# Kernel tuning notes

Hardware: AMD Instinct MI355X
Metric: run time of the kernel (lower is better)

The kernel has to match this reference:

```python
import jax, jax.numpy as jnp
import numpy as np

EPS = 1e-9
N_HEAD = 16


def clamp_c(c):
    return jnp.clip(c, 1e-4, 1.0)


def _heads(x, H):
    B, T, C = x.shape
    return x.reshape(B, T, H, C // H)


def mobius_add(x, y, c_clamped, H):
    # per-head Mobius addition; c_clamped: (H,)
    B, T, C = x.shape
    cr = c_clamped.reshape(1, 1, H, 1)
    xr, yr = _heads(x, H), _heads(y, H)
    xn = jnp.sum(xr * xr, axis=-1, keepdims=True)
    yn = jnp.sum(yr * yr, axis=-1, keepdims=True)
    ip = jnp.sum(xr * yr, axis=-1, keepdims=True)
    num = (1 + 2 * cr * ip + cr * yn) * xr + (1 - cr * xn) * yr
    den = 1 + 2 * cr * ip + cr ** 2 * xn * yn
    return (num / (den + EPS)).reshape(B, T, C)


def expmap(x, v, c, H):
    # exponential map of tangent vector v at point x (per-head curvature)
    B, T, C = x.shape
    cc = clamp_c(c)
    cr = cc.reshape(1, 1, H, 1)
    xr, vr = _heads(x, H), _heads(v, H)
    sf = 2.0 / (1 + cr * jnp.sum(xr * xr, axis=-1, keepdims=True) + EPS)  # scaling factor
    vns = jnp.sum(vr * vr, axis=-1, keepdims=True)
    vn = jnp.sqrt(vns + EPS)
    tanh_arg = jnp.abs(cr * sf * vns / 2)
    coeff = (1.0 / (jnp.sqrt(jnp.abs(cr) + EPS) + EPS)) * jnp.tanh(jnp.sqrt(tanh_arg + EPS))
    second = (coeff * vr / (vn + EPS)).reshape(B, T, C)
    return mobius_add(x, second, cc, H)


def layernorm(x, g):
    m = jnp.mean(x, axis=-1, keepdims=True)
    v = jnp.mean((x - m) ** 2, axis=-1, keepdims=True)
    return (x - m) * jax.lax.rsqrt(v + 1e-5) * g


def attention(x, w_qkv, w_proj, H):
    B, T, C = x.shape
    hs = C // H
    q, k, v = jnp.split(x @ w_qkv.T, 3, axis=-1)
    q = q.reshape(B, T, H, hs).transpose(0, 2, 1, 3)
    k = k.reshape(B, T, H, hs).transpose(0, 2, 1, 3)
    v = v.reshape(B, T, H, hs).transpose(0, 2, 1, 3)
    att = jnp.einsum('bhqd,bhkd->bhqk', q, k) * (float(hs) ** -0.5)
    mask = jnp.tril(jnp.ones((T, T), dtype=bool))
    att = jnp.where(mask, att, -jnp.inf)
    att = jax.nn.softmax(att, axis=-1)
    y = jnp.einsum('bhqk,bhkd->bhqd', att, v)
    y = y.transpose(0, 2, 1, 3).reshape(B, T, C)
    return y @ w_proj.T


def setup_inputs() -> dict:
    key = jax.random.key(0)
    ks = jax.random.split(key, 9)
    B, T, C = 2, 2048, 1024
    s = 0.02
    return {
        'x': jax.random.normal(ks[0], (B, T, C), jnp.float32) * s,
        'ln1_g': jnp.ones((C,), jnp.float32),
        'w_qkv': jax.random.normal(ks[1], (3 * C, C), jnp.float32) * s,
        'w_attn_proj': jax.random.normal(ks[2], (C, C), jnp.float32) * s,
        'c_attn': jax.random.uniform(ks[3], (N_HEAD,), jnp.float32, 0.1, 0.9),
        'ln2_g': jnp.ones((C,), jnp.float32),
        'w_fc': jax.random.normal(ks[4], (4 * C, C), jnp.float32) * s,
        'w_mlp_proj': jax.random.normal(ks[5], (C, 4 * C), jnp.float32) * s,
        'c_mlp': jax.random.uniform(ks[6], (N_HEAD,), jnp.float32, 0.1, 0.9),
    }


def reference(x, ln1_g, w_qkv, w_attn_proj, c_attn, ln2_g, w_fc, w_mlp_proj, c_mlp):
    H = N_HEAD
    a = attention(layernorm(x, ln1_g), w_qkv, w_attn_proj, H)
    x = expmap(x, a, c_attn, H)  # hyperbolic residual (attn)
    h = jax.nn.gelu(layernorm(x, ln2_g) @ w_fc.T, approximate=False) @ w_mlp_proj.T
    x = expmap(x, h, c_mlp, H)   # hyperbolic residual (mlp)
    return x
```

## Files before the change

### kernel.cpp

```cpp
#include <hip/hip_runtime.h>
#include <hip/hip_bf16.h>

typedef __attribute__((ext_vector_type(8))) short bf16x8;
typedef __attribute__((ext_vector_type(4))) float f32x4;

typedef const __attribute__((address_space(1))) void gv_t;
typedef __attribute__((address_space(3))) void lv_t;
#define GLL16(g, l) __builtin_amdgcn_global_load_lds((gv_t*)(g), (lv_t*)(l), 16, 0, 0)

#define WAITV8()  asm volatile("s_waitcnt vmcnt(8)" ::: "memory")
#define WAITV0()  asm volatile("s_waitcnt vmcnt(0)" ::: "memory")
#define WAITL0()  asm volatile("s_waitcnt lgkmcnt(0)" ::: "memory")
#define SCHEDB()  __builtin_amdgcn_sched_barrier(0)
#define BARRAW()  __builtin_amdgcn_s_barrier()

__device__ __forceinline__ short f2bf(float f) {
    __hip_bfloat16 h = __float2bfloat16(f);
    return *reinterpret_cast<short*>(&h);
}

__device__ __forceinline__ float wred(float v) {
    #pragma unroll
    for (int m = 1; m < 64; m <<= 1) v += __shfl_xor(v, m);
    return v;
}

__global__ __launch_bounds__(256) void cvt_kernel(const float* __restrict__ in,
                                                  short* __restrict__ out, int n4) {
    int i = blockIdx.x * 256 + threadIdx.x;
    if (i < n4) {
        float4 v = ((const float4*)in)[i];
        short4 o;
        o.x = f2bf(v.x); o.y = f2bf(v.y); o.z = f2bf(v.z); o.w = f2bf(v.w);
        ((short4*)out)[i] = o;
    }
}

__global__ __launch_bounds__(256) void ln_kernel(const float* __restrict__ x,
                                                 const float* __restrict__ g,
                                                 short* __restrict__ y) {
    const int row = blockIdx.x, tid = threadIdx.x;
    const float4 v = ((const float4*)(x + (size_t)row * 1024))[tid];
    float s = v.x + v.y + v.z + v.w;
    float s2 = v.x * v.x + v.y * v.y + v.z * v.z + v.w * v.w;
    #pragma unroll
    for (int m = 1; m < 64; m <<= 1) { s += __shfl_xor(s, m); s2 += __shfl_xor(s2, m); }
    __shared__ float rs[4], rs2[4];
    if ((tid & 63) == 0) { rs[tid >> 6] = s; rs2[tid >> 6] = s2; }
    __syncthreads();
    s = rs[0] + rs[1] + rs[2] + rs[3];
    s2 = rs2[0] + rs2[1] + rs2[2] + rs2[3];
    const float mean = s * (1.0f / 1024.0f);
    const float var = s2 * (1.0f / 1024.0f) - mean * mean;
    const float r = rsqrtf(var + 1e-5f);
    const float4 gg = ((const float4*)g)[tid];
    short4 o;
    o.x = f2bf((v.x - mean) * r * gg.x);
    o.y = f2bf((v.y - mean) * r * gg.y);
    o.z = f2bf((v.z - mean) * r * gg.z);
    o.w = f2bf((v.w - mean) * r * gg.w);
    ((short4*)y)[(size_t)row * 256 + tid] = o;
}

template <int EPI>
__global__ __launch_bounds__(256, 2) void gemm_bt(const short* __restrict__ A,
                                                  const short* __restrict__ Bw,
                                                  int M, int N, int LDK, int KL,
                                                  void* __restrict__ o0,
                                                  void* __restrict__ o1,
                                                  void* __restrict__ o2) {
    __shared__ __align__(16) short As[2][128 * 64];
    __shared__ __align__(16) short Bs[2][128 * 64];
    const int tid = threadIdx.x;
    const int wid = tid >> 6, lane = tid & 63;
    const int wm = wid >> 1, wn = wid & 1;
    const int col = lane & 15, grp = lane >> 4;
    const int r8 = lane >> 3, s8 = lane & 7;
    const int orig = blockIdx.x + (int)gridDim.x * blockIdx.y;
    const int xcd = orig & 7, idx = orig >> 3;
    const int NC = gridDim.y >> 2;
    const int mt = ((xcd >> 2) << 4) + (idx & 15);
    const int nt = (xcd & 3) * NC + (idx >> 4);
    const int m0 = mt * 128, n0 = nt * 128;
    const int z = blockIdx.z;
    f32x4 acc[4][4] = {};
    const short* ga = A + (size_t)m0 * LDK + (size_t)z * KL;
    const short* gb = Bw + (size_t)n0 * LDK + (size_t)z * KL;

#define GSTAGE(b_, t_) do {                                                     \
        const int k0_ = (t_) * 64;                                              \
        _Pragma("unroll")                                                       \
        for (int c = 0; c < 4; ++c) {                                           \
            const int row = c * 32 + wid * 8 + r8;                              \
            const int slot = s8 ^ (row & 7);                                    \
            GLL16(ga + (size_t)row * LDK + k0_ + slot * 8,                      \
                  (char*)&As[b_][0] + c * 4096 + wid * 1024);                   \
            GLL16(gb + (size_t)row * LDK + k0_ + slot * 8,                      \
                  (char*)&Bs[b_][0] + c * 4096 + wid * 1024);                   \
        }                                                                       \
    } while (0)

    const int NT = KL >> 6;
    GSTAGE(0, 0);
    if (NT > 1) { GSTAGE(1, 1); WAITV8(); } else { WAITV0(); }
    SCHEDB();
    BARRAW();
    int cur = 0;
    for (int t = 0; t < NT; ++t) {
        const char* At = (const char*)&As[cur][0];
        const char* Bt = (const char*)&Bs[cur][0];
        bf16x8 af[2][4], bfr[2][4];
        #pragma unroll
        for (int s = 0; s < 2; ++s)
            #pragma unroll
            for (int i = 0; i < 4; ++i) {
                const int rowA = wm * 64 + i * 16 + col;
                const int rowB = wn * 64 + i * 16 + col;
                af[s][i]  = *(const bf16x8*)(At + rowA * 128 + (((s * 4 + grp) ^ (rowA & 7)) << 4));
                bfr[s][i] = *(const bf16x8*)(Bt + rowB * 128 + (((s * 4 + grp) ^ (rowB & 7)) << 4));
            }
        WAITL0(); SCHEDB();
        BARRAW();
        if (t + 2 < NT) GSTAGE(cur, t + 2);
        #pragma unroll
        for (int s = 0; s < 2; ++s)
            #pragma unroll
            for (int mi = 0; mi < 4; ++mi)
                #pragma unroll
                for (int ni = 0; ni < 4; ++ni)
                    acc[mi][ni] = __builtin_amdgcn_mfma_f32_16x16x32_bf16(af[s][mi], bfr[s][ni], acc[mi][ni], 0, 0, 0);
        if (t + 1 < NT) {
            if (t + 2 < NT) { WAITV8(); } else { WAITV0(); }
            SCHEDB();
            BARRAW();
        }
        cur ^= 1;
    }
#undef GSTAGE
    #pragma unroll
    for (int mi = 0; mi < 4; ++mi) {
        #pragma unroll
        for (int ni = 0; ni < 4; ++ni) {
            #pragma unroll
            for (int i = 0; i < 4; ++i) {
                const int m = m0 + wm * 64 + mi * 16 + grp * 4 + i;
                const int n = n0 + wn * 64 + ni * 16 + col;
                const float v = acc[mi][ni][i];
                if (EPI == 0) {
                    const int b = m >> 11, t = m & 2047;
                    const int which = n >> 10, nn = n & 1023;
                    const int h = nn >> 6, d = nn & 63;
                    const size_t bh = (size_t)(b * 16 + h);
                    if (which == 0)
                        ((short*)o0)[(bh * 2048 + t) * 64 + d] = f2bf(v * 0.125f);
                    else if (which == 1)
                        ((short*)o1)[(bh * 2048 + t) * 64 + d] = f2bf(v);
                    else
                        ((short*)o2)[(bh * 64 + d) * 2048 + t] = f2bf(v);
                } else if (EPI == 1) {
                    float* dst = (z == 0) ? (float*)o0 : (float*)o1;
                    dst[(size_t)m * N + n] = v;
                } else {
                    const float gl = 0.5f * v * (1.0f + erff(v * 0.70710678118654752f));
                    ((short*)o0)[(size_t)m * N + n] = f2bf(gl);
                }
            }
        }
    }
}

__global__ __launch_bounds__(256, 3) void attn_kernel(const short* __restrict__ Q,
                                                      const short* __restrict__ Kg,
                                                      const short* __restrict__ VT,
                                                      short* __restrict__ Y) {
    __shared__ __align__(16) short Ks[2][4096];
    __shared__ __align__(16) short Vs[2][4096];
    __shared__ __align__(16) short Plds[4][16 * 72];
    const int j = 31 - blockIdx.x;
    const int bh = blockIdx.y;
    const int tid = threadIdx.x, wid = tid >> 6, lane = tid & 63;
    const int ql = lane & 15, g = lane >> 4;
    const int r8 = lane >> 3, s8 = lane & 7;
    const int q0s = j * 64 + wid * 16;
    const int lt = j;
    const short* Qb = Q + (size_t)bh * 2048 * 64;
    const short* Kb = Kg + (size_t)bh * 2048 * 64;
    const short* Vb = VT + (size_t)bh * 64 * 2048;
    short* Pw = &Plds[wid][0];

    bf16x8 qf0 = *(const bf16x8*)&Qb[(size_t)(q0s + ql) * 64 + 8 * g];
    bf16x8 qf1 = *(const bf16x8*)&Qb[(size_t)(q0s + ql) * 64 + 32 + 8 * g];
    f32x4 o[4] = {};
    float m = -1e30f, lsum = 0.0f;

#define STAGE(b_, kt_) do {                                                      \
        const int kbase_ = (kt_) * 64;                                           \
        _Pragma("unroll")                                                        \
        for (int c = 0; c < 2; ++c) {                                            \
            const int row = c * 32 + wid * 8 + r8;                               \
            const int slot = s8 ^ (row & 7);                                     \
            GLL16(Kb + (size_t)(kbase_ + row) * 64 + slot * 8,                   \
                  (char*)&Ks[b_][0] + c * 4096 + wid * 1024);                    \
            GLL16(Vb + (size_t)row * 2048 + kbase_ + slot * 8,                   \
                  (char*)&Vs[b_][0] + c * 4096 + wid * 1024);                    \
        }                                                                        \
    } while (0)

    STAGE(0, 0);
    __syncthreads();
    int buf = 0;
    for (int kt = 0; kt <= lt; ++kt) {
        if (kt < lt) STAGE(buf ^ 1, kt + 1);
        const int kbase = kt * 64;
        const short* Kt = &Ks[buf][0];
        const short* Vt = &Vs[buf][0];
        bf16x8 kf[4][2];
        #pragma unroll
        for (int kb = 0; kb < 4; ++kb) {
            const int row = 16 * kb + ql;
            const int x = row & 7;
            kf[kb][0] = *(const bf16x8*)((const char*)Kt + row * 128 + ((g ^ x) << 4));
            kf[kb][1] = *(const bf16x8*)((const char*)Kt + row * 128 + (((4 + g) ^ x) << 4));
        }
        f32x4 s[4];
        #pragma unroll
        for (int kb = 0; kb < 4; ++kb) {
            f32x4 z = {0.f, 0.f, 0.f, 0.f};
            z = __builtin_amdgcn_mfma_f32_16x16x32_bf16(kf[kb][0], qf0, z, 0, 0, 0);
            z = __builtin_amdgcn_mfma_f32_16x16x32_bf16(kf[kb][1], qf1, z, 0, 0, 0);
            s[kb] = z;
        }
        if (kbase + 63 > q0s) {
            #pragma unroll
            for (int kb = 0; kb < 4; ++kb)
                #pragma unroll
                for (int r = 0; r < 4; ++r)
                    if (kbase + 16 * kb + 4 * g + r > q0s + ql) s[kb][r] = -1e30f;
        }
        float t0 = fmaxf(fmaxf(s[0][0], s[0][1]), fmaxf(s[0][2], s[0][3]));
        float t1 = fmaxf(fmaxf(s[1][0], s[1][1]), fmaxf(s[1][2], s[1][3]));
        float t2 = fmaxf(fmaxf(s[2][0], s[2][1]), fmaxf(s[2][2], s[2][3]));
        float t3 = fmaxf(fmaxf(s[3][0], s[3][1]), fmaxf(s[3][2], s[3][3]));
        float tmax = fmaxf(fmaxf(t0, t1), fmaxf(t2, t3));
        tmax = fmaxf(tmax, __shfl_xor(tmax, 16));
        tmax = fmaxf(tmax, __shfl_xor(tmax, 32));
        const float mnew = fmaxf(m, tmax);
        const float sc = __expf(m - mnew);
        m = mnew;
        float rsum = 0.0f;
        #pragma unroll
        for (int kb = 0; kb < 4; ++kb) {
            const float e0 = __expf(s[kb][0] - mnew);
            const float e1 = __expf(s[kb][1] - mnew);
            const float e2 = __expf(s[kb][2] - mnew);
            const float e3 = __expf(s[kb][3] - mnew);
            rsum += (e0 + e1) + (e2 + e3);
            short4 pk;
            pk.x = f2bf(e0); pk.y = f2bf(e1); pk.z = f2bf(e2); pk.w = f2bf(e3);
            *(short4*)&Pw[ql * 72 + 16 * kb + 4 * g] = pk;
        }
        rsum += __shfl_xor(rsum, 16);
        rsum += __shfl_xor(rsum, 32);
        lsum = lsum * sc + rsum;
        #pragma unroll
        for (int nf = 0; nf < 4; ++nf)
            #pragma unroll
            for (int r = 0; r < 4; ++r) o[nf][r] *= sc;
        const bf16x8 pb0 = *(const bf16x8*)&Pw[ql * 72 + 8 * g];
        const bf16x8 pb1 = *(const bf16x8*)&Pw[ql * 72 + 32 + 8 * g];
        #pragma unroll
        for (int nf = 0; nf < 4; ++nf) {
            const int row = 16 * nf + ql;
            const int x = row & 7;
            bf16x8 v0 = *(const bf16x8*)((const char*)Vt + row * 128 + ((g ^ x) << 4));
            bf16x8 v1 = *(const bf16x8*)((const char*)Vt + row * 128 + (((4 + g) ^ x) << 4));
            o[nf] = __builtin_amdgcn_mfma_f32_16x16x32_bf16(v0, pb0, o[nf], 0, 0, 0);
            o[nf] = __builtin_amdgcn_mfma_f32_16x16x32_bf16(v1, pb1, o[nf], 0, 0, 0);
        }
        __syncthreads();
        buf ^= 1;
    }
#undef STAGE
    const int b = bh >> 4, h = bh & 15;
    const float inv = 1.0f / lsum;
    const size_t rowoff = ((size_t)b * 2048 + q0s + ql) * 1024 + h * 64;
    #pragma unroll
    for (int nf = 0; nf < 4; ++nf) {
        short4 w;
        w.x = f2bf(o[nf][0] * inv);
        w.y = f2bf(o[nf][1] * inv);
        w.z = f2bf(o[nf][2] * inv);
        w.w = f2bf(o[nf][3] * inv);
        *(short4*)&Y[rowoff + 16 * nf + 4 * g] = w;
    }
}

__global__ __launch_bounds__(256) void expmap_kernel(const float* __restrict__ x,
                                                     const float* __restrict__ va,
                                                     const float* __restrict__ vb,
                                                     const float* __restrict__ carr,
                                                     float* __restrict__ out) {
    const int blk = blockIdx.x;
    const int row = blk >> 2;
    const int head = (blk & 3) * 4 + (threadIdx.x >> 6);
    const int lane = threadIdx.x & 63;
    const size_t idx = (size_t)row * 1024 + head * 64 + lane;
    float c = carr[head];
    c = fminf(fmaxf(c, 1e-4f), 1.0f);
    const float xe = x[idx], ve = va[idx] + vb[idx];
    const float xn = wred(xe * xe);
    const float vns = wred(ve * ve);
    const float vn = sqrtf(vns + 1e-9f);
    const float sf = 2.0f / (1.0f + c * xn + 1e-9f);
    const float targ = fabsf(0.5f * c * sf * vns);
    const float coeff = (1.0f / (sqrtf(c + 1e-9f) + 1e-9f)) * tanhf(sqrtf(targ + 1e-9f));
    const float ye = coeff * ve / (vn + 1e-9f);
    const float yn = wred(ye * ye);
    const float ip = wred(xe * ye);
    const float num = (1.0f + 2.0f * c * ip + c * yn) * xe + (1.0f - c * xn) * ye;
    const float den = 1.0f + 2.0f * c * ip + c * c * xn * yn;
    out[idx] = num / (den + 1e-9f);
}

extern "C" void kernel_launch(void* const* d_in, const int* in_sizes, int n_in,
                              void* d_out, int out_size, void* d_ws, size_t ws_size,
                              hipStream_t stream) {
    (void)in_sizes; (void)n_in; (void)out_size; (void)ws_size;
    const float* x      = (const float*)d_in[0];
    const float* ln1_g  = (const float*)d_in[1];
    const float* w_qkv  = (const float*)d_in[2];
    const float* w_proj = (const float*)d_in[3];
    const float* c_attn = (const float*)d_in[4];
    const float* ln2_g  = (const float*)d_in[5];
    const float* w_fc   = (const float*)d_in[6];
    const float* w_mlp  = (const float*)d_in[7];
    const float* c_mlp  = (const float*)d_in[8];
    float* out = (float*)d_out;
    char* ws = (char*)d_ws;
    const size_t MB = 1024 * 1024;

    short* wqkv_bf  = (short*)(ws + 0 * MB);
    short* wproj_bf = (short*)(ws + 6 * MB);
    short* wfc_bf   = (short*)(ws + 8 * MB);
    short* wmlp_bf  = (short*)(ws + 16 * MB);
    short* y_bf     = (short*)(ws + 24 * MB);
    short* q_bf     = (short*)(ws + 32 * MB);
    short* k_bf     = (short*)(ws + 40 * MB);
    short* vT_bf    = (short*)(ws + 48 * MB);
    short* att_bf   = (short*)(ws + 56 * MB);
    float* a0       = (float*)(ws + 64 * MB);
    float* a1       = (float*)(ws + 80 * MB);
    float* x1       = (float*)(ws + 40 * MB);
    short* g_bf     = (short*)(ws + 56 * MB);
    float* h0       = (float*)(ws + 0 * MB);
    float* h1       = (float*)(ws + 24 * MB);

    cvt_kernel<<<3072, 256, 0, stream>>>(w_qkv, wqkv_bf, 3072 * 1024 / 4);
    cvt_kernel<<<1024, 256, 0, stream>>>(w_proj, wproj_bf, 1024 * 1024 / 4);
    cvt_kernel<<<4096, 256, 0, stream>>>(w_fc, wfc_bf, 4096 * 1024 / 4);
    cvt_kernel<<<4096, 256, 0, stream>>>(w_mlp, wmlp_bf, 1024 * 4096 / 4);

    ln_kernel<<<4096, 256, 0, stream>>>(x, ln1_g, y_bf);
    gemm_bt<0><<<dim3(32, 24, 1), 256, 0, stream>>>(y_bf, wqkv_bf, 4096, 3072, 1024, 1024,
                                                    q_bf, k_bf, vT_bf);
    attn_kernel<<<dim3(32, 32), 256, 0, stream>>>(q_bf, k_bf, vT_bf, att_bf);
    gemm_bt<1><<<dim3(32, 8, 2), 256, 0, stream>>>(att_bf, wproj_bf, 4096, 1024, 1024, 512,
                                                   a0, a1, nullptr);
    expmap_kernel<<<16384, 256, 0, stream>>>(x, a0, a1, c_attn, x1);
    ln_kernel<<<4096, 256, 0, stream>>>(x1, ln2_g, y_bf);
    gemm_bt<2><<<dim3(32, 32, 1), 256, 0, stream>>>(y_bf, wfc_bf, 4096, 4096, 1024, 1024,
                                                    g_bf, nullptr, nullptr);
    gemm_bt<1><<<dim3(32, 8, 2), 256, 0, stream>>>(g_bf, wmlp_bf, 4096, 1024, 4096, 2048,
                                                   h0, h1, nullptr);
    expmap_kernel<<<16384, 256, 0, stream>>>(x1, h0, h1, c_mlp, out);
}
```

Baseline: 299.4 us.

## Add 256x256-tile GEMM kernel for QKV and FC projections

```diff
diff --git a/kernel.cpp b/kernel.cpp
--- a/kernel.cpp
+++ b/kernel.cpp
@@ -63,6 +63,123 @@
 }
 
 template <int EPI>
+__global__ __launch_bounds__(512, 2) void gemm256(const short* __restrict__ A,
+                                                  const short* __restrict__ Bw,
+                                                  int M, int N, int LDK, int KL,
+                                                  void* __restrict__ o0,
+                                                  void* __restrict__ o1,
+                                                  void* __restrict__ o2) {
+    __shared__ __align__(16) short As[2][256 * 64];
+    __shared__ __align__(16) short Bs[2][256 * 64];
+    const int tid = threadIdx.x;
+    const int wid = tid >> 6, lane = tid & 63;
+    const int wm = wid >> 2, wn = wid & 3;
+    const int col = lane & 15, grp = lane >> 4;
+    const int r8 = lane >> 3, s8 = lane & 7;
+    const int m0 = blockIdx.x * 256, n0 = blockIdx.y * 256;
+    f32x4 acc[8][4] = {};
+    const short* ga = A + (size_t)m0 * LDK;
+    const short* gb = Bw + (size_t)n0 * LDK;
+
+#define GSTAGE(b_, t_) do {                                                     \
+        const int k0_ = (t_) * 64;                                              \
+        _Pragma("unroll")                                                       \
+        for (int c = 0; c < 4; ++c) {                                           \
+            const int row = c * 64 + wid * 8 + r8;                              \
+            const int slot = s8 ^ (row & 7);                                    \
+            GLL16(ga + (size_t)row * LDK + k0_ + slot * 8,                      \
+                  (char*)&As[b_][0] + c * 8192 + wid * 1024);                   \
+            GLL16(gb + (size_t)row * LDK + k0_ + slot * 8,                      \
+                  (char*)&Bs[b_][0] + c * 8192 + wid * 1024);                   \
+        }                                                                       \
+    } while (0)
+
+    const int NT = KL >> 6;
+    GSTAGE(0, 0);
+    GSTAGE(1, 1);
+    WAITV8(); SCHEDB();
+    BARRAW();
+    int cur = 0;
+    for (int t = 0; t < NT; ++t) {
+        const char* At = (const char*)&As[cur][0];
+        const char* Bt = (const char*)&Bs[cur][0];
+        {
+            bf16x8 af[8], bfr[4];
+            #pragma unroll
+            for (int i = 0; i < 8; ++i) {
+                const int rowA = wm * 128 + i * 16 + col;
+                af[i] = *(const bf16x8*)(At + rowA * 128 + ((grp ^ (rowA & 7)) << 4));
+            }
+            #pragma unroll
+            for (int j = 0; j < 4; ++j) {
+                const int rowB = wn * 64 + j * 16 + col;
+                bfr[j] = *(const bf16x8*)(Bt + rowB * 128 + ((grp ^ (rowB & 7)) << 4));
+            }
+            #pragma unroll
+            for (int mi = 0; mi < 8; ++mi)
+                #pragma unroll
+                for (int nj = 0; nj < 4; ++nj)
+                    acc[mi][nj] = __builtin_amdgcn_mfma_f32_16x16x32_bf16(af[mi], bfr[nj], acc[mi][nj], 0, 0, 0);
+        }
+        {
+            bf16x8 af[8], bfr[4];
+            #pragma unroll
+            for (int i = 0; i < 8; ++i) {
+                const int rowA = wm * 128 + i * 16 + col;
+                af[i] = *(const bf16x8*)(At + rowA * 128 + (((4 + grp) ^ (rowA & 7)) << 4));
+            }
+            #pragma unroll
+            for (int j = 0; j < 4; ++j) {
+                const int rowB = wn * 64 + j * 16 + col;
+                bfr[j] = *(const bf16x8*)(Bt + rowB * 128 + (((4 + grp) ^ (rowB & 7)) << 4));
+            }
+            WAITL0(); SCHEDB();
+            BARRAW();
+            if (t + 2 < NT) GSTAGE(cur, t + 2);
+            #pragma unroll
+            for (int mi = 0; mi < 8; ++mi)
+                #pragma unroll
+                for (int nj = 0; nj < 4; ++nj)
+                    acc[mi][nj] = __builtin_amdgcn_mfma_f32_16x16x32_bf16(af[mi], bfr[nj], acc[mi][nj], 0, 0, 0);
+        }
+        if (t + 1 < NT) {
+            if (t + 2 < NT) { WAITV8(); } else { WAITV0(); }
+            SCHEDB();
+            BARRAW();
+        }
+        cur ^= 1;
+    }
+#undef GSTAGE
+    #pragma unroll
+    for (int mi = 0; mi < 8; ++mi) {
+        #pragma unroll
+        for (int nj = 0; nj < 4; ++nj) {
+            #pragma unroll
+            for (int i = 0; i < 4; ++i) {
+                const int m = m0 + wm * 128 + mi * 16 + grp * 4 + i;
+                const int n = n0 + wn * 64 + nj * 16 + col;
+                const float v = acc[mi][nj][i];
+                if (EPI == 0) {
+                    const int b = m >> 11, t = m & 2047;
+                    const int which = n >> 10, nn = n & 1023;
+                    const int h = nn >> 6, d = nn & 63;
+                    const size_t bh = (size_t)(b * 16 + h);
+                    if (which == 0)
+                        ((short*)o0)[(bh * 2048 + t) * 64 + d] = f2bf(v * 0.125f);
+                    else if (which == 1)
+                        ((short*)o1)[(bh * 2048 + t) * 64 + d] = f2bf(v);
+                    else
+                        ((short*)o2)[(bh * 64 + d) * 2048 + t] = f2bf(v);
+                } else {
+                    const float gl = 0.5f * v * (1.0f + erff(v * 0.70710678118654752f));
+                    ((short*)o0)[(size_t)m * N + n] = f2bf(gl);
+                }
+            }
+        }
+    }
+}
+
+template <int EPI>
 __global__ __launch_bounds__(256, 2) void gemm_bt(const short* __restrict__ A,
                                                   const short* __restrict__ Bw,
                                                   int M, int N, int LDK, int KL,
@@ -146,18 +263,7 @@
                 const int m = m0 + wm * 64 + mi * 16 + grp * 4 + i;
                 const int n = n0 + wn * 64 + ni * 16 + col;
                 const float v = acc[mi][ni][i];
-                if (EPI == 0) {
-                    const int b = m >> 11, t = m & 2047;
-                    const int which = n >> 10, nn = n & 1023;
-                    const int h = nn >> 6, d = nn & 63;
-                    const size_t bh = (size_t)(b * 16 + h);
-                    if (which == 0)
-                        ((short*)o0)[(bh * 2048 + t) * 64 + d] = f2bf(v * 0.125f);
-                    else if (which == 1)
-                        ((short*)o1)[(bh * 2048 + t) * 64 + d] = f2bf(v);
-                    else
-                        ((short*)o2)[(bh * 64 + d) * 2048 + t] = f2bf(v);
-                } else if (EPI == 1) {
+                if (EPI == 1) {
                     float* dst = (z == 0) ? (float*)o0 : (float*)o1;
                     dst[(size_t)m * N + n] = v;
                 } else {
@@ -361,15 +467,15 @@
     cvt_kernel<<<4096, 256, 0, stream>>>(w_mlp, wmlp_bf, 1024 * 4096 / 4);
 
     ln_kernel<<<4096, 256, 0, stream>>>(x, ln1_g, y_bf);
-    gemm_bt<0><<<dim3(32, 24, 1), 256, 0, stream>>>(y_bf, wqkv_bf, 4096, 3072, 1024, 1024,
-                                                    q_bf, k_bf, vT_bf);
+    gemm256<0><<<dim3(16, 12), 512, 0, stream>>>(y_bf, wqkv_bf, 4096, 3072, 1024, 1024,
+                                                 q_bf, k_bf, vT_bf);
     attn_kernel<<<dim3(32, 32), 256, 0, stream>>>(q_bf, k_bf, vT_bf, att_bf);
     gemm_bt<1><<<dim3(32, 8, 2), 256, 0, stream>>>(att_bf, wproj_bf, 4096, 1024, 1024, 512,
                                                    a0, a1, nullptr);
     expmap_kernel<<<16384, 256, 0, stream>>>(x, a0, a1, c_attn, x1);
     ln_kernel<<<4096, 256, 0, stream>>>(x1, ln2_g, y_bf);
-    gemm_bt<2><<<dim3(32, 32, 1), 256, 0, stream>>>(y_bf, wfc_bf, 4096, 4096, 1024, 1024,
-                                                    g_bf, nullptr, nullptr);
+    gemm256<2><<<dim3(16, 16), 512, 0, stream>>>(y_bf, wfc_bf, 4096, 4096, 1024, 1024,
+                                                 g_bf, nullptr, nullptr);
     gemm_bt<1><<<dim3(32, 8, 2), 256, 0, stream>>>(g_bf, wmlp_bf, 4096, 1024, 4096, 2048,
                                                    h0, h1, nullptr);
     expmap_kernel<<<16384, 256, 0, stream>>>(x1, h0, h1, c_mlp, out);
```

After: 334.5 us. 1.12x slower.

## Add 256x256-tile 8-wave ping-pong GEMM for QKV and FC projections

Applied to the files above, without the earlier changes.

```diff
diff --git a/kernel.cpp b/kernel.cpp
--- a/kernel.cpp
+++ b/kernel.cpp
@@ -9,6 +9,7 @@
 #define GLL16(g, l) __builtin_amdgcn_global_load_lds((gv_t*)(g), (lv_t*)(l), 16, 0, 0)
 
 #define WAITV8()  asm volatile("s_waitcnt vmcnt(8)" ::: "memory")
+#define WAITV4()  asm volatile("s_waitcnt vmcnt(4)" ::: "memory")
 #define WAITV0()  asm volatile("s_waitcnt vmcnt(0)" ::: "memory")
 #define WAITL0()  asm volatile("s_waitcnt lgkmcnt(0)" ::: "memory")
 #define SCHEDB()  __builtin_amdgcn_sched_barrier(0)
@@ -23,6 +24,11 @@
     #pragma unroll
     for (int m = 1; m < 64; m <<= 1) v += __shfl_xor(v, m);
     return v;
+}
+
+__device__ __forceinline__ bf16x8 ldsfrag(const short* buf, int rin, int slot) {
+    const int s = slot ^ (rin & 7);
+    return *(const bf16x8*)((const char*)buf + rin * 128 + (s << 4));
 }
 
 __global__ __launch_bounds__(256) void cvt_kernel(const float* __restrict__ in,
@@ -63,6 +69,150 @@
 }
 
 template <int EPI>
+__global__ __launch_bounds__(512) void gemm8p(const short* __restrict__ A,
+                                              const short* __restrict__ Bw,
+                                              int M, int N, int LDK,
+                                              void* __restrict__ o0,
+                                              void* __restrict__ o1,
+                                              void* __restrict__ o2) {
+    __shared__ __align__(16) short As[2][2][128 * 64];
+    __shared__ __align__(16) short Bs[2][2][128 * 64];
+    const int tid = threadIdx.x;
+    const int wid = tid >> 6, lane = tid & 63;
+    const int wm = wid >> 2, wn = wid & 3;
+    const int col = lane & 15, grp = lane >> 4;
+    const int r8 = lane >> 3, s8 = lane & 7;
+    const int m0 = blockIdx.x * 256, n0 = blockIdx.y * 256;
+    f32x4 acc[8][4] = {};
+    const short* ga = A + (size_t)m0 * LDK;
+    const short* gb = Bw + (size_t)n0 * LDK;
+    const short* myA[2] = { &As[0][wm][0], &As[1][wm][0] };
+    const short* myB[2] = { &Bs[0][wn >> 1][0], &Bs[1][wn >> 1][0] };
+    const int brow = (wn & 1) * 64;
+    const int NT = LDK >> 6;
+
+#define STAGE_HALF(G_, rbase_, k0_, ldsbuf_) do {                               \
+        _Pragma("unroll")                                                       \
+        for (int c = 0; c < 2; ++c) {                                           \
+            const int row = c * 64 + wid * 8 + r8;                              \
+            const int slot = s8 ^ (row & 7);                                    \
+            GLL16((G_) + (size_t)((rbase_) + row) * LDK + (k0_) + slot * 8,     \
+                  (char*)(ldsbuf_) + c * 8192 + wid * 1024);                    \
+        }                                                                       \
+    } while (0)
+
+#define READ_A(dsel, mibase)                                                    \
+        _Pragma("unroll")                                                       \
+        for (int j = 0; j < 2; ++j) {                                           \
+            af[j][0] = ldsfrag(myA[dsel], (mibase + j) * 16 + col, grp);        \
+            af[j][1] = ldsfrag(myA[dsel], (mibase + j) * 16 + col, 4 + grp);    \
+        }
+
+#define READ_B(dsel)                                                            \
+        _Pragma("unroll")                                                       \
+        for (int nj = 0; nj < 4; ++nj) {                                        \
+            bf[nj][0] = ldsfrag(myB[dsel], brow + nj * 16 + col, grp);          \
+            bf[nj][1] = ldsfrag(myB[dsel], brow + nj * 16 + col, 4 + grp);      \
+        }
+
+#define DO_MFMA(mibase)                                                         \
+        __builtin_amdgcn_s_setprio(1);                                          \
+        _Pragma("unroll")                                                       \
+        for (int ks = 0; ks < 2; ++ks)                                          \
+            _Pragma("unroll")                                                   \
+            for (int j = 0; j < 2; ++j)                                         \
+                _Pragma("unroll")                                               \
+                for (int nj = 0; nj < 4; ++nj)                                  \
+                    acc[mibase + j][nj] = __builtin_amdgcn_mfma_f32_16x16x32_bf16( \
+                        af[j][ks], bf[nj][ks], acc[mibase + j][nj], 0, 0, 0);   \
+        __builtin_amdgcn_s_setprio(0);
+
+#define PHASE_SYNC_IN()  SCHEDB(); BARRAW(); WAITL0(); SCHEDB()
+#define PHASE_SYNC_OUT() SCHEDB(); BARRAW()
+
+    STAGE_HALF(ga, 0,   0,  &As[0][0][0]);
+    STAGE_HALF(ga, 128, 0,  &As[0][1][0]);
+    STAGE_HALF(gb, 0,   0,  &Bs[0][0][0]);
+    STAGE_HALF(gb, 128, 0,  &Bs[0][1][0]);
+    STAGE_HALF(gb, 0,   64, &Bs[1][0][0]);
+    STAGE_HALF(gb, 128, 64, &Bs[1][1][0]);
+    WAITV4(); SCHEDB();
+    BARRAW();
+
+    const int NIT = NT >> 1;
+    for (int it = 0; it < NIT; ++it) {
+        const int t1k = (2 * it + 1) << 6;
+        const int t2k = (2 * it + 2) << 6;
+        const int t3k = (2 * it + 3) << 6;
+        const bool h2 = (2 * it + 2) < NT;
+        const bool h3 = (2 * it + 3) < NT;
+        bf16x8 bf[4][2], af[2][2];
+
+        READ_B(0) READ_A(0, 0)
+        STAGE_HALF(ga, 0, t1k, &As[1][0][0]);
+        PHASE_SYNC_IN(); DO_MFMA(0) PHASE_SYNC_OUT();
+        READ_A(0, 2)
+        STAGE_HALF(ga, 128, t1k, &As[1][1][0]);
+        PHASE_SYNC_IN(); DO_MFMA(2) PHASE_SYNC_OUT();
+        READ_A(0, 4)
+        if (h2) STAGE_HALF(gb, 0, t2k, &Bs[0][0][0]);
+        PHASE_SYNC_IN(); DO_MFMA(4) PHASE_SYNC_OUT();
+        READ_A(0, 6)
+        if (h2) STAGE_HALF(gb, 128, t2k, &Bs[0][1][0]);
+        PHASE_SYNC_IN(); DO_MFMA(6)
+        if (h2) { WAITV4(); } else { WAITV0(); }
+        PHASE_SYNC_OUT();
+        READ_B(1) READ_A(1, 0)
+        if (h2) STAGE_HALF(ga, 0, t2k, &As[0][0][0]);
+        PHASE_SYNC_IN(); DO_MFMA(0) PHASE_SYNC_OUT();
+        READ_A(1, 2)
+        if (h2) STAGE_HALF(ga, 128, t2k, &As[0][1][0]);
+        PHASE_SYNC_IN(); DO_MFMA(2) PHASE_SYNC_OUT();
+        READ_A(1, 4)
+        if (h3) STAGE_HALF(gb, 0, t3k, &Bs[1][0][0]);
+        PHASE_SYNC_IN(); DO_MFMA(4) PHASE_SYNC_OUT();
+        READ_A(1, 6)
+        if (h3) STAGE_HALF(gb, 128, t3k, &Bs[1][1][0]);
+        PHASE_SYNC_IN(); DO_MFMA(6)
+        if (h3) { WAITV4(); } else { WAITV0(); }
+        PHASE_SYNC_OUT();
+    }
+#undef STAGE_HALF
+#undef READ_A
+#undef READ_B
+#undef DO_MFMA
+#undef PHASE_SYNC_IN
+#undef PHASE_SYNC_OUT
+    #pragma unroll
+    for (int mi = 0; mi < 8; ++mi) {
+        #pragma unroll
+        for (int nj = 0; nj < 4; ++nj) {
+            #pragma unroll
+            for (int i = 0; i < 4; ++i) {
+                const int m = m0 + wm * 128 + mi * 16 + grp * 4 + i;
+                const int n = n0 + wn * 64 + nj * 16 + col;
+                const float v = acc[mi][nj][i];
+                if (EPI == 0) {
+                    const int b = m >> 11, t = m & 2047;
+                    const int which = n >> 10, nn = n & 1023;
+                    const int h = nn >> 6, d = nn & 63;
+                    const size_t bh = (size_t)(b * 16 + h);
+                    if (which == 0)
+                        ((short*)o0)[(bh * 2048 + t) * 64 + d] = f2bf(v * 0.125f);
+                    else if (which == 1)
+                        ((short*)o1)[(bh * 2048 + t) * 64 + d] = f2bf(v);
+                    else
+                        ((short*)o2)[(bh * 64 + d) * 2048 + t] = f2bf(v);
+                } else {
+                    const float gl = 0.5f * v * (1.0f + erff(v * 0.70710678118654752f));
+                    ((short*)o0)[(size_t)m * N + n] = f2bf(gl);
+                }
+            }
+        }
+    }
+}
+
+template <int EPI>
 __global__ __launch_bounds__(256, 2) void gemm_bt(const short* __restrict__ A,
                                                   const short* __restrict__ Bw,
                                                   int M, int N, int LDK, int KL,
@@ -146,18 +296,7 @@
                 const int m = m0 + wm * 64 + mi * 16 + grp * 4 + i;
                 const int n = n0 + wn * 64 + ni * 16 + col;
                 const float v = acc[mi][ni][i];
-                if (EPI == 0) {
-                    const int b = m >> 11, t = m & 2047;
-                    const int which = n >> 10, nn = n & 1023;
-                    const int h = nn >> 6, d = nn & 63;
-                    const size_t bh = (size_t)(b * 16 + h);
-                    if (which == 0)
-                        ((short*)o0)[(bh * 2048 + t) * 64 + d] = f2bf(v * 0.125f);
-                    else if (which == 1)
-                        ((short*)o1)[(bh * 2048 + t) * 64 + d] = f2bf(v);
-                    else
-                        ((short*)o2)[(bh * 64 + d) * 2048 + t] = f2bf(v);
-                } else if (EPI == 1) {
+                if (EPI == 1) {
                     float* dst = (z == 0) ? (float*)o0 : (float*)o1;
                     dst[(size_t)m * N + n] = v;
                 } else {
@@ -361,15 +500,15 @@
     cvt_kernel<<<4096, 256, 0, stream>>>(w_mlp, wmlp_bf, 1024 * 4096 / 4);
 
     ln_kernel<<<4096, 256, 0, stream>>>(x, ln1_g, y_bf);
-    gemm_bt<0><<<dim3(32, 24, 1), 256, 0, stream>>>(y_bf, wqkv_bf, 4096, 3072, 1024, 1024,
-                                                    q_bf, k_bf, vT_bf);
+    gemm8p<0><<<dim3(16, 12), 512, 0, stream>>>(y_bf, wqkv_bf, 4096, 3072, 1024,
+                                                q_bf, k_bf, vT_bf);
     attn_kernel<<<dim3(32, 32), 256, 0, stream>>>(q_bf, k_bf, vT_bf, att_bf);
     gemm_bt<1><<<dim3(32, 8, 2), 256, 0, stream>>>(att_bf, wproj_bf, 4096, 1024, 1024, 512,
                                                    a0, a1, nullptr);
     expmap_kernel<<<16384, 256, 0, stream>>>(x, a0, a1, c_attn, x1);
     ln_kernel<<<4096, 256, 0, stream>>>(x1, ln2_g, y_bf);
-    gemm_bt<2><<<dim3(32, 32, 1), 256, 0, stream>>>(y_bf, wfc_bf, 4096, 4096, 1024, 1024,
-                                                    g_bf, nullptr, nullptr);
+    gemm8p<2><<<dim3(16, 16), 512, 0, stream>>>(y_bf, wfc_bf, 4096, 4096, 1024,
+                                                g_bf, nullptr, nullptr);
     gemm_bt<1><<<dim3(32, 8, 2), 256, 0, stream>>>(g_bf, wmlp_bf, 4096, 1024, 4096, 2048,
                                                    h0, h1, nullptr);
     expmap_kernel<<<16384, 256, 0, stream>>>(x1, h0, h1, c_mlp, out);
```

Result: slower. 343.3 us (+14.7%).
